# Performance work log

Hardware: AMD Instinct MI355X
Metric: run time of the kernel (lower is better)

## Reference

```python
import jax, jax.numpy as jnp
import numpy as np

N_NODES = 100000
N_QUERIES = 128
D = 128
E = 131072

def leaky(x):
    return jax.nn.leaky_relu(x, negative_slope=0.01)

def setup_inputs() -> dict:
    key = jax.random.key(0)
    ks = jax.random.split(key, 16)
    inp = {
        'visited_node_score': jax.random.uniform(ks[0], (N_NODES,), jnp.float32),
        'node_rep': jax.random.normal(ks[1], (N_NODES, D), jnp.float32),
        'query_src_ts_emb': jax.random.normal(ks[2], (N_QUERIES, D), jnp.float32),
        'query_rel_emb': jax.random.normal(ks[3], (N_QUERIES, D), jnp.float32),
        'rel_emb': jax.random.normal(ks[4], (E, D), jnp.float32),
        'W_left': jax.random.normal(ks[5], (2 * D, 4 * D), jnp.float32) * np.sqrt(2.0 / (4 * D)),
        'b_left': jnp.zeros((2 * D,), jnp.float32),
        'W_right': jax.random.normal(ks[6], (2 * D, 4 * D), jnp.float32) * np.sqrt(2.0 / (4 * D)),
        'b_right': jnp.zeros((2 * D,), jnp.float32),
        'W_center': jax.random.normal(ks[7], (2 * D, 2 * D), jnp.float32) * np.sqrt(2.0 / (4 * D)),
        'b_center': jnp.zeros((2 * D,), jnp.float32),
        'W_step': jax.random.normal(ks[8], (D, D), jnp.float32) * np.sqrt(2.0 / (2 * D)),
        'b_step': jnp.zeros((D,), jnp.float32),
        'query_idx': jax.random.randint(ks[9], (E,), 0, N_QUERIES, jnp.int32),
        'idx_i': jax.random.randint(ks[10], (E,), 0, N_NODES, jnp.int32),
        'idx_j': jax.random.randint(ks[11], (E,), 0, N_NODES, jnp.int32),
        'max_edges': 1024,
    }
    return inp

def _forward(visited_node_score, node_rep, query_src_ts_emb, query_rel_emb, rel_emb,
             W_left, b_left, W_right, b_right, W_center, b_center, W_step, b_step,
             query_idx, idx_i, idx_j, max_edges):
    num_nodes = node_rep.shape[0]
    num_q = query_src_ts_emb.shape[0]
    e = rel_emb.shape[0]
    # gathers (irregular access)
    hi = node_rep[idx_i]            # [E, D]
    hj = node_rep[idx_j]            # [E, D]
    qs = query_src_ts_emb[query_idx]  # [E, D]
    qr = query_rel_emb[query_idx]     # [E, D]
    # G bilinear module: sum(leaky(L x) * C(leaky(R y)), -1)
    left_x = jnp.concatenate([hi, rel_emb, qs, qr], axis=-1)   # [E, 4D]
    right_x = jnp.concatenate([hj, rel_emb, qs, qr], axis=-1)  # [E, 4D]
    l = leaky(left_x @ W_left.T + b_left)                      # [E, 2D]
    r = leaky(right_x @ W_right.T + b_right) @ W_center.T + b_center  # [E, 2D]
    logits = jnp.sum(l * r, axis=-1)                           # [E]
    # segment softmax over source node idx (idx_i), as segment_softmax_op_v2
    seg_max = jax.ops.segment_max(logits, idx_i, num_segments=num_nodes)
    ex = jnp.exp(logits - seg_max[idx_i])
    denom = jax.ops.segment_sum(ex, idx_i, num_segments=num_nodes)
    attn = ex / denom[idx_i]                                   # [E]
    src_score = visited_node_score[idx_i]
    target_score = attn * src_score                            # [E]
    # per-query-group top-k pruning (mask instead of dynamic-shape slice)
    order = jnp.lexsort((-target_score, query_idx))            # sort by group, score desc
    g_sorted = query_idx[order]
    pos = jnp.arange(e, dtype=jnp.int32)
    starts = jax.ops.segment_min(pos, g_sorted, num_segments=num_q)
    rank_sorted = pos - starts[g_sorted]
    rank = jnp.zeros((e,), jnp.int32).at[order].set(rank_sorted)
    keep = (rank < max_edges).astype(logits.dtype)             # [E]
    # sum aggregation of pruned target scores into target nodes (sparse mm)
    updated_node_score = jax.ops.segment_sum(keep * target_score, idx_j, num_segments=num_nodes)
    # update node representation along pruned edges (attention-weighted message passing)
    attn_pruned = keep * attn
    agg = jax.ops.segment_sum(attn_pruned[:, None] * hi, idx_j, num_segments=num_nodes)
    new_rep = node_rep + agg
    # bypass_forward: linear_between_steps + LeakyReLU
    out_rep = leaky(new_rep @ W_step.T + b_step)
    return updated_node_score, out_rep

def reference(visited_node_score, node_rep, query_src_ts_emb, query_rel_emb, rel_emb,
              W_left, b_left, W_right, b_right, W_center, b_center, W_step, b_step,
              query_idx, idx_i, idx_j, max_edges):
    return _forward(visited_node_score, node_rep, query_src_ts_emb, query_rel_emb, rel_emb,
                    W_left, b_left, W_right, b_right, W_center, b_center, W_step, b_step,
                    query_idx, idx_i, idx_j, max_edges)
```

## Files before the change

### kernel.cpp

```cpp
#include <hip/hip_runtime.h>

typedef unsigned short u16;
typedef unsigned int   u32;
typedef __attribute__((ext_vector_type(8))) short short8;
typedef __attribute__((ext_vector_type(4))) short short4v;
typedef __attribute__((ext_vector_type(4))) float f32x4;

#define N_NODES 100000
#define NQ      128
#define DD      128
#define NE      131072
#define OO      256

__device__ __forceinline__ float b2f(u16 b){ u32 u = ((u32)b) << 16; return __uint_as_float(u); }
__device__ __forceinline__ u16 f2b(float f){ u32 u = __float_as_uint(f); u32 r = (u + 0x7FFFu + ((u >> 16) & 1u)) >> 16; return (u16)r; }
__device__ __forceinline__ float lrelu(float x){ return x > 0.0f ? x : 0.01f * x; }
__device__ __forceinline__ u32 fenc(float f){ u32 u = __float_as_uint(f); return (u & 0x80000000u) ? ~u : (u | 0x80000000u); }
__device__ __forceinline__ float fdec(u32 e){ u32 u = (e & 0x80000000u) ? (e & 0x7FFFFFFFu) : ~e; return __uint_as_float(u); }

__device__ __forceinline__ void stage4(f32x4 v, u16* dhi, u16* dlo){
  short4v h4, l4;
  #pragma unroll
  for (int i = 0; i < 4; ++i){
    u16 h = f2b(v[i]); h4[i] = (short)h; l4[i] = (short)f2b(v[i] - b2f(h));
  }
  *(short4v*)dhi = h4; *(short4v*)dlo = l4;
}

__global__ void split_kernel(const float* __restrict__ src, u16* __restrict__ hi,
                             u16* __restrict__ lo, int n)
{
  int i = blockIdx.x*256 + threadIdx.x; if (i >= n) return;
  float x = src[i];
  u16 h = f2b(x);
  hi[i] = h;
  lo[i] = f2b(x - b2f(h));
}

__global__ __launch_bounds__(256) void qtable_kernel(
    const float* __restrict__ qsrc, const float* __restrict__ qrel,
    const float* __restrict__ Wl, const float* __restrict__ bl,
    const float* __restrict__ Wr, const float* __restrict__ br,
    float* __restrict__ Qlt, float* __restrict__ Qrt)
{
  int b = blockIdx.x; int side = b >> 7; int q = b & 127; int o = threadIdx.x;
  __shared__ __align__(16) float s[2*DD];
  if (threadIdx.x < DD) s[threadIdx.x] = qsrc[q*DD + threadIdx.x];
  else                  s[threadIdx.x] = qrel[q*DD + threadIdx.x - DD];
  __syncthreads();
  const float* W    = side ? Wr : Wl;
  const float* bias = side ? br : bl;
  float acc = bias[o];
  const float* wrow = W + (size_t)o*512 + 256;
  #pragma unroll 4
  for (int k4 = 0; k4 < 64; ++k4){
    f32x4 wv = *(const f32x4*)(wrow + k4*4);
    f32x4 sv = *(const f32x4*)(s + k4*4);
    acc += sv[0]*wv[0]; acc += sv[1]*wv[1]; acc += sv[2]*wv[2]; acc += sv[3]*wv[3];
  }
  (side ? Qrt : Qlt)[q*OO + o] = acc;
}

#define BM   64
#define RSTc 264
#define HST  136

template<int WS, int PF>
__device__ __forceinline__ void gemm8(f32x4 (&ACC)[4][2],
    const u16* __restrict__ WH, const u16* __restrict__ WL,
    const u16* A0H, const u16* A0L, const u16* A1H, const u16* A1L, int ASTR,
    int ow, int ln, int qd)
{
  short8 nbh[2], nbl[2];
  if (PF){
    #pragma unroll
    for (int nt = 0; nt < 2; ++nt){ int o = ow + nt*16 + ln;
      nbh[nt] = *(const short8*)(WH + (size_t)o*WS + qd*8);
      nbl[nt] = *(const short8*)(WL + (size_t)o*WS + qd*8);
    }
  }
  #pragma unroll
  for (int c = 0; c < 8; ++c){
    short8 bh[2], bl[2], ah[4], al[4];
    if (PF){
      #pragma unroll
      for (int nt = 0; nt < 2; ++nt){ bh[nt] = nbh[nt]; bl[nt] = nbl[nt]; }
      if (c < 7){
        #pragma unroll
        for (int nt = 0; nt < 2; ++nt){ int o = ow + nt*16 + ln;
          nbh[nt] = *(const short8*)(WH + (size_t)o*WS + (c+1)*32 + qd*8);
          nbl[nt] = *(const short8*)(WL + (size_t)o*WS + (c+1)*32 + qd*8);
        }
      }
    } else {
      #pragma unroll
      for (int nt = 0; nt < 2; ++nt){ int o = ow + nt*16 + ln;
        bh[nt] = *(const short8*)(WH + (size_t)o*WS + c*32 + qd*8);
        bl[nt] = *(const short8*)(WL + (size_t)o*WS + c*32 + qd*8);
      }
    }
    const u16* hs = (c < 4) ? A0H : A1H;
    const u16* ls = (c < 4) ? A0L : A1L;
    int cc = (c < 4) ? c : c - 4;
    #pragma unroll
    for (int mt = 0; mt < 4; ++mt){
      int base = (mt*16 + ln)*ASTR + cc*32 + qd*8;
      ah[mt] = *(const short8*)&hs[base];
      al[mt] = *(const short8*)&ls[base];
    }
    #pragma unroll
    for (int mt = 0; mt < 4; ++mt)
      #pragma unroll
      for (int nt = 0; nt < 2; ++nt)
        ACC[mt][nt] = __builtin_amdgcn_mfma_f32_16x16x32_bf16(ah[mt], bh[nt], ACC[mt][nt], 0, 0, 0);
    #pragma unroll
    for (int mt = 0; mt < 4; ++mt)
      #pragma unroll
      for (int nt = 0; nt < 2; ++nt)
        ACC[mt][nt] = __builtin_amdgcn_mfma_f32_16x16x32_bf16(ah[mt], bl[nt], ACC[mt][nt], 0, 0, 0);
    #pragma unroll
    for (int mt = 0; mt < 4; ++mt)
      #pragma unroll
      for (int nt = 0; nt < 2; ++nt)
        ACC[mt][nt] = __builtin_amdgcn_mfma_f32_16x16x32_bf16(al[mt], bh[nt], ACC[mt][nt], 0, 0, 0);
  }
}

__global__ __launch_bounds__(512, 4) void edge_logits_kernel(
    const float* __restrict__ node_rep, const float* __restrict__ rel_emb,
    const u16* __restrict__ WlH, const u16* __restrict__ WlL,
    const u16* __restrict__ WrH, const u16* __restrict__ WrL,
    const u16* __restrict__ WcH, const u16* __restrict__ WcL,
    const float* __restrict__ bcb,
    const float* __restrict__ Qlt, const float* __restrict__ Qrt,
    const int* __restrict__ idx_i, const int* __restrict__ idx_j, const int* __restrict__ qidx,
    float* __restrict__ logits, u32* __restrict__ segmax, int* __restrict__ qcount)
{
  __shared__ __align__(16) u16 bufA[2*BM*HST];
  __shared__ __align__(16) u16 bufB[2*BM*HST];
  __shared__ int qidS[BM];
  __shared__ float lpart[8][BM];

  u16* HjHi = bufA;  u16* HjLo = bufA + BM*HST;
  u16* ReHi = bufB;  u16* ReLo = bufB + BM*HST;
  u16* RRhi = bufA;  u16* RRlo = bufB;

  const int tid = threadIdx.x;
  const int e0 = blockIdx.x * BM;
  const int lane = tid & 63, w = tid >> 6;
  const int ln = lane & 15, qd = lane >> 4;
  const int ow = w * 32;

  if (tid < BM) qidS[tid] = qidx[e0 + tid];

  #pragma unroll
  for (int it = 0; it < 4; ++it){
    int c = tid + it*512;
    int r = c >> 5, seg = (c & 31) << 2;
    int j = idx_j[e0 + r];
    f32x4 vj = *(const f32x4*)(node_rep + (size_t)j*DD + seg);
    f32x4 vr = *(const f32x4*)(rel_emb + (size_t)(e0 + r)*DD + seg);
    stage4(vj, &HjHi[r*HST + seg], &HjLo[r*HST + seg]);
    stage4(vr, &ReHi[r*HST + seg], &ReLo[r*HST + seg]);
  }
  f32x4 hipre[4];
  #pragma unroll
  for (int it = 0; it < 4; ++it){
    int c = tid + it*512;
    int r = c >> 5, seg = (c & 31) << 2;
    hipre[it] = *(const f32x4*)(node_rep + (size_t)idx_i[e0 + r]*DD + seg);
  }
  __syncthreads();

  f32x4 acc[4][2];
  #pragma unroll
  for (int mt = 0; mt < 4; ++mt)
    #pragma unroll
    for (int nt = 0; nt < 2; ++nt) acc[mt][nt] = (f32x4){0.f,0.f,0.f,0.f};
  gemm8<512, 1>(acc, WrH, WrL, HjHi, HjLo, ReHi, ReLo, HST, ow, ln, qd);
  __syncthreads();

  #pragma unroll
  for (int it = 0; it < 4; ++it){
    int c = tid + it*512;
    int r = c >> 5, seg = (c & 31) << 2;
    stage4(hipre[it], &HjHi[r*HST + seg], &HjLo[r*HST + seg]);
  }
  __syncthreads();

  f32x4 lacc[4][2];
  #pragma unroll
  for (int mt = 0; mt < 4; ++mt)
    #pragma unroll
    for (int nt = 0; nt < 2; ++nt) lacc[mt][nt] = (f32x4){0.f,0.f,0.f,0.f};
  gemm8<512, 0>(lacc, WlH, WlL, HjHi, HjLo, ReHi, ReLo, HST, ow, ln, qd);
  __syncthreads();

  #pragma unroll
  for (int mt = 0; mt < 4; ++mt)
    #pragma unroll
    for (int nt = 0; nt < 2; ++nt){
      int col = ow + nt*16 + ln;
      #pragma unroll
      for (int rg = 0; rg < 4; ++rg){
        int row = mt*16 + qd*4 + rg;
        float v = acc[mt][nt][rg] + Qrt[qidS[row]*OO + col];
        v = lrelu(v);
        u16 hi = f2b(v);
        RRhi[row*RSTc + col] = hi;
        RRlo[row*RSTc + col] = f2b(v - b2f(hi));
      }
    }
  __syncthreads();

  f32x4 racc[4][2];
  #pragma unroll
  for (int mt = 0; mt < 4; ++mt)
    #pragma unroll
    for (int nt = 0; nt < 2; ++nt) racc[mt][nt] = (f32x4){0.f,0.f,0.f,0.f};
  gemm8<256, 1>(racc, WcH, WcL, RRhi, RRlo, RRhi + 128, RRlo + 128, RSTc, ow, ln, qd);

  float bcv[2];
  #pragma unroll
  for (int nt = 0; nt < 2; ++nt) bcv[nt] = bcb[ow + nt*16 + ln];

  float part[4][4];
  #pragma unroll
  for (int mt = 0; mt < 4; ++mt)
    #pragma unroll
    for (int rg = 0; rg < 4; ++rg) part[mt][rg] = 0.f;

  #pragma unroll
  for (int mt = 0; mt < 4; ++mt)
    #pragma unroll
    for (int nt = 0; nt < 2; ++nt){
      int col = ow + nt*16 + ln;
      #pragma unroll
      for (int rg = 0; rg < 4; ++rg){
        int row = mt*16 + qd*4 + rg;
        float lv = lacc[mt][nt][rg] + Qlt[qidS[row]*OO + col];
        lv = lrelu(lv);
        float rv = racc[mt][nt][rg] + bcv[nt];
        part[mt][rg] += lv * rv;
      }
    }

  #pragma unroll
  for (int mt = 0; mt < 4; ++mt)
    #pragma unroll
    for (int rg = 0; rg < 4; ++rg){
      float p = part[mt][rg];
      p += __shfl_xor(p, 1); p += __shfl_xor(p, 2);
      p += __shfl_xor(p, 4); p += __shfl_xor(p, 8);
      if (ln == 0) lpart[w][mt*16 + qd*4 + rg] = p;
    }
  __syncthreads();
  if (tid < BM){
    float lg = lpart[0][tid] + lpart[1][tid] + lpart[2][tid] + lpart[3][tid]
             + lpart[4][tid] + lpart[5][tid] + lpart[6][tid] + lpart[7][tid];
    int e = e0 + tid;
    logits[e] = lg;
    atomicMax(segmax + idx_i[e], fenc(lg));
    atomicAdd(qcount + qidx[e], 1);
  }
}

__global__ void seg_exp_sum_kernel(const float* __restrict__ logits,
    const int* __restrict__ idx_i, const u32* __restrict__ segmax,
    float* __restrict__ ex, float* __restrict__ denom)
{
  int e = blockIdx.x*256 + threadIdx.x; if (e >= NE) return;
  int i = idx_i[e];
  float d = fminf(logits[e] - fdec(segmax[i]), 0.0f);
  float v = expf(d);
  ex[e] = v;
  atomicAdd(denom + i, v);
}

__global__ void scan_kernel(const int* __restrict__ qcount,
                            int* __restrict__ qstart, int* __restrict__ qcursor)
{
  if (blockIdx.x == 0 && threadIdx.x == 0){
    int acc = 0;
    for (int i = 0; i < NQ; ++i){ qstart[i] = acc; qcursor[i] = acc; acc += qcount[i]; }
  }
}

__global__ void attn_bucket_kernel(const float* __restrict__ ex,
    const float* __restrict__ denom, const int* __restrict__ idx_i,
    const float* __restrict__ visited, const int* __restrict__ qidx,
    int* __restrict__ qcursor, int* __restrict__ bucket,
    float* __restrict__ attn, float* __restrict__ target)
{
  int e = blockIdx.x*256 + threadIdx.x; if (e >= NE) return;
  int i = idx_i[e];
  float a = ex[e] / fmaxf(denom[i], 1e-30f);
  attn[e] = a;
  target[e] = a * visited[i];
  int p = atomicAdd(qcursor + qidx[e], 1);
  bucket[p] = e;
}

#define TOPK_CAP 2560
__global__ __launch_bounds__(1024) void topk_kernel(
    const int* __restrict__ qcount, const int* __restrict__ qstart,
    const int* __restrict__ bucket, const float* __restrict__ target,
    const int* __restrict__ maxe_p, int* __restrict__ keep)
{
  __shared__ float ss[TOPK_CAP];
  __shared__ int   se[TOPK_CAP];
  int q = blockIdx.x;
  int m = qcount[q], start = qstart[q];
  int maxe = *maxe_p;
  if (maxe <= 0 || maxe > (1 << 30)){
    float f = __int_as_float(maxe);
    if (f > 0.0f && f < 1.0e9f) maxe = (int)f;
  }
  int tid = threadIdx.x;
  if (m <= maxe){
    for (int i = tid; i < m; i += 1024) keep[bucket[start + i]] = 1;
    return;
  }
  if (m <= TOPK_CAP){
    for (int i = tid; i < m; i += 1024){
      int e = bucket[start + i]; ss[i] = target[e]; se[i] = e;
    }
    __syncthreads();
    for (int i = tid; i < m; i += 1024){
      float s = ss[i]; int eid = se[i]; int cnt = 0;
      for (int j = 0; j < m; ++j){
        float sj = ss[j]; int ej = se[j];
        cnt += (sj > s) || (sj == s && ej < eid);
      }
      keep[eid] = (cnt < maxe) ? 1 : 0;
    }
  } else {
    for (int i = tid; i < m; i += 1024){
      int eid = bucket[start + i]; float s = target[eid]; int cnt = 0;
      for (int j = 0; j < m; ++j){
        int ej = bucket[start + j]; float sj = target[ej];
        cnt += (sj > s) || (sj == s && ej < eid);
      }
      keep[eid] = (cnt < maxe) ? 1 : 0;
    }
  }
}

__global__ __launch_bounds__(256) void edge_scatter_kernel(
    const int* __restrict__ keep, const float* __restrict__ attn,
    const float* __restrict__ target,
    const int* __restrict__ idx_i, const int* __restrict__ idx_j,
    const float* __restrict__ node_rep,
    float* __restrict__ out_score, float* __restrict__ agg)
{
  int wid = (blockIdx.x * 256 + threadIdx.x) >> 6;
  if (wid >= NE) return;
  if (!keep[wid]) return;
  int lane = threadIdx.x & 63;
  int ii = idx_i[wid], jj = idx_j[wid];
  float a = attn[wid];
  if (lane == 0) atomicAdd(out_score + jj, target[wid]);
  float h0 = node_rep[(size_t)ii*DD + lane];
  float h1 = node_rep[(size_t)ii*DD + 64 + lane];
  atomicAdd(agg + (size_t)jj*DD + lane,      a*h0);
  atomicAdd(agg + (size_t)jj*DD + 64 + lane, a*h1);
}

__global__ __launch_bounds__(256) void final_mfma_kernel(
    const float* __restrict__ node_rep, const float* __restrict__ aggc,
    const u16* __restrict__ WsH, const u16* __restrict__ WsL,
    const float* __restrict__ bstep, float* __restrict__ out_rep)
{
  __shared__ __align__(16) u16 Ahi[64*HST];
  __shared__ __align__(16) u16 Alo[64*HST];
  const int tid = threadIdx.x;
  const int m0 = blockIdx.x * 64;

  for (int c = tid; c < 64*32; c += 256){
    int r = c >> 5, seg = (c & 31) << 2;
    int m = m0 + r;
    float v[4];
    if (m < N_NODES){
      const float* nr = node_rep + (size_t)m*DD + seg;
      const float* ag = aggc + (size_t)m*DD + seg;
      #pragma unroll
      for (int i = 0; i < 4; ++i) v[i] = nr[i] + ag[i];
    } else {
      #pragma unroll
      for (int i = 0; i < 4; ++i) v[i] = 0.f;
    }
    short4v h4, l4;
    #pragma unroll
    for (int i = 0; i < 4; ++i){
      u16 h = f2b(v[i]); h4[i] = (short)h; l4[i] = (short)f2b(v[i] - b2f(h));
    }
    *(short4v*)&Ahi[r*HST + seg] = h4;
    *(short4v*)&Alo[r*HST + seg] = l4;
  }
  __syncthreads();

  const int lane = tid & 63, w = tid >> 6;
  const int ln = lane & 15, qd = lane >> 4;
  const int ow = w * 32;

  short8 bh[2][4], bl[2][4];
  #pragma unroll
  for (int nt = 0; nt < 2; ++nt)
    #pragma unroll
    for (int c = 0; c < 4; ++c){
      int o = ow + nt*16 + ln;
      bh[nt][c] = *(const short8*)(WsH + (size_t)o*DD + c*32 + qd*8);
      bl[nt][c] = *(const short8*)(WsL + (size_t)o*DD + c*32 + qd*8);
    }

  f32x4 acc[4][2];
  #pragma unroll
  for (int mt = 0; mt < 4; ++mt)
    #pragma unroll
    for (int nt = 0; nt < 2; ++nt) acc[mt][nt] = (f32x4){0.f,0.f,0.f,0.f};

  #pragma unroll
  for (int mt = 0; mt < 4; ++mt)
    #pragma unroll
    for (int c = 0; c < 4; ++c){
      int base = (mt*16 + ln)*HST + c*32 + qd*8;
      short8 ah = *(const short8*)&Ahi[base];
      short8 al = *(const short8*)&Alo[base];
      #pragma unroll
      for (int nt = 0; nt < 2; ++nt){
        acc[mt][nt] = __builtin_amdgcn_mfma_f32_16x16x32_bf16(ah, bh[nt][c], acc[mt][nt], 0, 0, 0);
        acc[mt][nt] = __builtin_amdgcn_mfma_f32_16x16x32_bf16(ah, bl[nt][c], acc[mt][nt], 0, 0, 0);
        acc[mt][nt] = __builtin_amdgcn_mfma_f32_16x16x32_bf16(al, bh[nt][c], acc[mt][nt], 0, 0, 0);
      }
    }

  #pragma unroll
  for (int mt = 0; mt < 4; ++mt)
    #pragma unroll
    for (int nt = 0; nt < 2; ++nt){
      int col = ow + nt*16 + ln;
      float bs = bstep[col];
      #pragma unroll
      for (int rg = 0; rg < 4; ++rg){
        int m = m0 + mt*16 + qd*4 + rg;
        if (m < N_NODES)
          out_rep[(size_t)m*DD + col] = lrelu(acc[mt][nt][rg] + bs);
      }
    }
}

extern "C" void kernel_launch(void* const* d_in, const int* in_sizes, int n_in,
                              void* d_out, int out_size, void* d_ws, size_t ws_size,
                              hipStream_t stream)
{
  const float* visited  = (const float*)d_in[0];
  const float* node_rep = (const float*)d_in[1];
  const float* qsrc     = (const float*)d_in[2];
  const float* qrel     = (const float*)d_in[3];
  const float* rel_emb  = (const float*)d_in[4];
  const float* Wl       = (const float*)d_in[5];
  const float* bl       = (const float*)d_in[6];
  const float* Wr       = (const float*)d_in[7];
  const float* br       = (const float*)d_in[8];
  const float* Wc       = (const float*)d_in[9];
  const float* bcb      = (const float*)d_in[10];
  const float* Wstep    = (const float*)d_in[11];
  const float* bstep    = (const float*)d_in[12];
  const int* qidx       = (const int*)d_in[13];
  const int* idx_i      = (const int*)d_in[14];
  const int* idx_j      = (const int*)d_in[15];
  const int* maxe       = (const int*)d_in[16];

  char* wp = (char*)d_ws;
  size_t used = 0;
  auto alloc = [&](size_t bytes)->char*{
    size_t pad = (bytes + 255) & ~(size_t)255;
    char* p = wp + used; used += pad; return p;
  };
  float* Qlt    = (float*)alloc((size_t)NQ*OO*4);
  float* Qrt    = (float*)alloc((size_t)NQ*OO*4);
  float* logits = (float*)alloc((size_t)NE*4);
  float* ex     = (float*)alloc((size_t)NE*4);
  float* attn   = (float*)alloc((size_t)NE*4);
  float* target = (float*)alloc((size_t)NE*4);
  u32*   segmax = (u32*)  alloc((size_t)N_NODES*4);
  float* denom  = (float*)alloc((size_t)N_NODES*4);
  int*   qcount = (int*)  alloc((size_t)NQ*4);
  int*   qstart = (int*)  alloc((size_t)NQ*4);
  int*   qcursor= (int*)  alloc((size_t)NQ*4);
  int*   bucket = (int*)  alloc((size_t)NE*4);
  int*   keep   = (int*)  alloc((size_t)NE*4);
  u16* WlH = (u16*)alloc((size_t)256*512*2); u16* WlL = (u16*)alloc((size_t)256*512*2);
  u16* WrH = (u16*)alloc((size_t)256*512*2); u16* WrL = (u16*)alloc((size_t)256*512*2);
  u16* WcH = (u16*)alloc((size_t)256*256*2); u16* WcL = (u16*)alloc((size_t)256*256*2);
  u16* WsH = (u16*)alloc((size_t)128*128*2); u16* WsL = (u16*)alloc((size_t)128*128*2);
  (void)ws_size; (void)in_sizes; (void)n_in; (void)out_size;

  float* out_score = (float*)d_out;
  float* out_rep   = (float*)d_out + N_NODES;

  hipMemsetAsync(d_out, 0, ((size_t)N_NODES + (size_t)N_NODES*DD)*4, stream);
  hipMemsetAsync(segmax, 0, (size_t)N_NODES*4, stream);
  hipMemsetAsync(denom,  0, (size_t)N_NODES*4, stream);
  hipMemsetAsync(qcount, 0, (size_t)NQ*4,      stream);
  hipMemsetAsync(keep,   0, (size_t)NE*4,      stream);

  split_kernel<<<(256*512+255)/256, 256, 0, stream>>>(Wl, WlH, WlL, 256*512);
  split_kernel<<<(256*512+255)/256, 256, 0, stream>>>(Wr, WrH, WrL, 256*512);
  split_kernel<<<(256*256+255)/256, 256, 0, stream>>>(Wc, WcH, WcL, 256*256);
  split_kernel<<<(128*128+255)/256, 256, 0, stream>>>(Wstep, WsH, WsL, 128*128);

  qtable_kernel<<<256, 256, 0, stream>>>(qsrc, qrel, Wl, bl, Wr, br, Qlt, Qrt);

  edge_logits_kernel<<<NE/BM, 512, 0, stream>>>(node_rep, rel_emb,
      WlH, WlL, WrH, WrL, WcH, WcL, bcb, Qlt, Qrt, idx_i, idx_j, qidx,
      logits, segmax, qcount);

  seg_exp_sum_kernel<<<NE/256, 256, 0, stream>>>(logits, idx_i, segmax, ex, denom);
  scan_kernel<<<1, 64, 0, stream>>>(qcount, qstart, qcursor);
  attn_bucket_kernel<<<NE/256, 256, 0, stream>>>(ex, denom, idx_i, visited, qidx,
                                                 qcursor, bucket, attn, target);
  topk_kernel<<<NQ, 1024, 0, stream>>>(qcount, qstart, bucket, target, maxe, keep);

  edge_scatter_kernel<<<NE/4, 256, 0, stream>>>(keep, attn, target, idx_i, idx_j,
                                                node_rep, out_score, out_rep);
  final_mfma_kernel<<<(N_NODES + 63)/64, 256, 0, stream>>>(node_rep, out_rep,
                                               WsH, WsL, bstep, out_rep);
}
```

Before: 845.2 us.

## Merge weight split launches, parallelize query scan, prestage hi bf16 split

Four separate weight-splitting launches become one kernel that dispatches on a flat index. The single-thread serial prefix scan over query counts is replaced by a 128-thread shared-memory Hillis-Steele scan. In the edge kernel, the gathered hi rows are converted to bf16 hi/lo pairs in registers before the first GEMM, so the later stage only stores them, which also trims register footprint. The second GEMM's template flag changes from 0 to 1, which may alter its loading or accumulation path and carries a correctness risk if that flag has semantic meaning.

```diff
diff --git a/kernel.cpp b/kernel.cpp
--- a/kernel.cpp
+++ b/kernel.cpp
@@ -27,14 +27,36 @@
   *(short4v*)dhi = h4; *(short4v*)dlo = l4;
 }
 
-__global__ void split_kernel(const float* __restrict__ src, u16* __restrict__ hi,
-                             u16* __restrict__ lo, int n)
-{
-  int i = blockIdx.x*256 + threadIdx.x; if (i >= n) return;
-  float x = src[i];
+__device__ __forceinline__ void cvt4(f32x4 v, short4v& h4, short4v& l4){
+  #pragma unroll
+  for (int i = 0; i < 4; ++i){
+    u16 h = f2b(v[i]); h4[i] = (short)h; l4[i] = (short)f2b(v[i] - b2f(h));
+  }
+}
+
+#define SPL_N1 (256*512)
+#define SPL_N2 (256*512)
+#define SPL_N3 (256*256)
+#define SPL_N4 (128*128)
+__global__ void split_all_kernel(
+    const float* __restrict__ Wl, const float* __restrict__ Wr,
+    const float* __restrict__ Wc, const float* __restrict__ Ws,
+    u16* __restrict__ WlH, u16* __restrict__ WlL,
+    u16* __restrict__ WrH, u16* __restrict__ WrL,
+    u16* __restrict__ WcH, u16* __restrict__ WcL,
+    u16* __restrict__ WsH, u16* __restrict__ WsL)
+{
+  int i = blockIdx.x*256 + threadIdx.x;
+  const float* src; u16 *hi, *lo; int k = i;
+  if (k < SPL_N1){ src = Wl; hi = WlH; lo = WlL; }
+  else if ((k -= SPL_N1) < SPL_N2){ src = Wr; hi = WrH; lo = WrL; }
+  else if ((k -= SPL_N2) < SPL_N3){ src = Wc; hi = WcH; lo = WcL; }
+  else if ((k -= SPL_N3) < SPL_N4){ src = Ws; hi = WsH; lo = WsL; }
+  else return;
+  float x = src[k];
   u16 h = f2b(x);
-  hi[i] = h;
-  lo[i] = f2b(x - b2f(h));
+  hi[k] = h;
+  lo[k] = f2b(x - b2f(h));
 }
 
 __global__ __launch_bounds__(256) void qtable_kernel(
@@ -163,12 +185,13 @@
     stage4(vj, &HjHi[r*HST + seg], &HjLo[r*HST + seg]);
     stage4(vr, &ReHi[r*HST + seg], &ReLo[r*HST + seg]);
   }
-  f32x4 hipre[4];
+  short4v hpreH[4], hpreL[4];
   #pragma unroll
   for (int it = 0; it < 4; ++it){
     int c = tid + it*512;
     int r = c >> 5, seg = (c & 31) << 2;
-    hipre[it] = *(const f32x4*)(node_rep + (size_t)idx_i[e0 + r]*DD + seg);
+    f32x4 v = *(const f32x4*)(node_rep + (size_t)idx_i[e0 + r]*DD + seg);
+    cvt4(v, hpreH[it], hpreL[it]);
   }
   __syncthreads();
 
@@ -184,7 +207,8 @@
   for (int it = 0; it < 4; ++it){
     int c = tid + it*512;
     int r = c >> 5, seg = (c & 31) << 2;
-    stage4(hipre[it], &HjHi[r*HST + seg], &HjLo[r*HST + seg]);
+    *(short4v*)&HjHi[r*HST + seg] = hpreH[it];
+    *(short4v*)&HjLo[r*HST + seg] = hpreL[it];
   }
   __syncthreads();
 
@@ -193,7 +217,7 @@
   for (int mt = 0; mt < 4; ++mt)
     #pragma unroll
     for (int nt = 0; nt < 2; ++nt) lacc[mt][nt] = (f32x4){0.f,0.f,0.f,0.f};
-  gemm8<512, 0>(lacc, WlH, WlL, HjHi, HjLo, ReHi, ReLo, HST, ow, ln, qd);
+  gemm8<512, 1>(lacc, WlH, WlL, HjHi, HjLo, ReHi, ReLo, HST, ow, ln, qd);
   __syncthreads();
 
   #pragma unroll
@@ -277,13 +301,24 @@
   atomicAdd(denom + i, v);
 }
 
-__global__ void scan_kernel(const int* __restrict__ qcount,
+__global__ __launch_bounds__(128) void scan_kernel(const int* __restrict__ qcount,
                             int* __restrict__ qstart, int* __restrict__ qcursor)
 {
-  if (blockIdx.x == 0 && threadIdx.x == 0){
-    int acc = 0;
-    for (int i = 0; i < NQ; ++i){ qstart[i] = acc; qcursor[i] = acc; acc += qcount[i]; }
-  }
+  __shared__ int s[NQ];
+  int t = threadIdx.x;
+  int mine = qcount[t];
+  s[t] = mine;
+  __syncthreads();
+  #pragma unroll
+  for (int off = 1; off < NQ; off <<= 1){
+    int v = (t >= off) ? s[t - off] : 0;
+    __syncthreads();
+    s[t] += v;
+    __syncthreads();
+  }
+  int excl = s[t] - mine;
+  qstart[t] = excl;
+  qcursor[t] = excl;
 }
 
 __global__ void attn_bucket_kernel(const float* __restrict__ ex,
@@ -505,10 +540,11 @@
   hipMemsetAsync(qcount, 0, (size_t)NQ*4,      stream);
   hipMemsetAsync(keep,   0, (size_t)NE*4,      stream);
 
-  split_kernel<<<(256*512+255)/256, 256, 0, stream>>>(Wl, WlH, WlL, 256*512);
-  split_kernel<<<(256*512+255)/256, 256, 0, stream>>>(Wr, WrH, WrL, 256*512);
-  split_kernel<<<(256*256+255)/256, 256, 0, stream>>>(Wc, WcH, WcL, 256*256);
-  split_kernel<<<(128*128+255)/256, 256, 0, stream>>>(Wstep, WsH, WsL, 128*128);
+  {
+    int n_all = SPL_N1 + SPL_N2 + SPL_N3 + SPL_N4;
+    split_all_kernel<<<(n_all + 255)/256, 256, 0, stream>>>(Wl, Wr, Wc, Wstep,
+        WlH, WlL, WrH, WrL, WcH, WcL, WsH, WsL);
+  }
 
   qtable_kernel<<<256, 256, 0, stream>>>(qsrc, qrel, Wl, bl, Wr, br, Qlt, Qrt);
 
@@ -517,7 +553,7 @@
       logits, segmax, qcount);
 
   seg_exp_sum_kernel<<<NE/256, 256, 0, stream>>>(logits, idx_i, segmax, ex, denom);
-  scan_kernel<<<1, 64, 0, stream>>>(qcount, qstart, qcursor);
+  scan_kernel<<<1, 128, 0, stream>>>(qcount, qstart, qcursor);
   attn_bucket_kernel<<<NE/256, 256, 0, stream>>>(ex, denom, idx_i, visited, qidx,
                                                  qcursor, bucket, attn, target);
   topk_kernel<<<NQ, 1024, 0, stream>>>(qcount, qstart, bucket, target, maxe, keep);
```

After: 841.2 us (median of 2 runs). Within noise of the previous version (-0.5%).
